# Performance work log

Measured on AMD Instinct MI355X. Metric: run time of the kernel, lower is better.

The kernel has to match this reference:

```python
import jax, jax.numpy as jnp
import numpy as np
from jax import lax

CONF_T = 0.25   # NMS.conf
IOU_T = 0.45    # NMS.iou
MAX_DET = 1000  # NMS.max_det
K_PRE = 1024    # fixed pre-NMS candidate count (static-shape surrogate for boolean filtering)
MAX_WH = 4096.0 # class offset for class-aware NMS (yolov5 trick)


def _xywh2xyxy(b):
    xy, wh = b[..., :2], b[..., 2:4]
    return jnp.concatenate([xy - wh * 0.5, xy + wh * 0.5], axis=-1)


def _box_iou(a, b):
    # a: [K,4], b: [K,4] xyxy -> [K,K]
    area_a = (a[:, 2] - a[:, 0]) * (a[:, 3] - a[:, 1])
    area_b = (b[:, 2] - b[:, 0]) * (b[:, 3] - b[:, 1])
    lt = jnp.maximum(a[:, None, :2], b[None, :, :2])
    rb = jnp.minimum(a[:, None, 2:], b[None, :, 2:])
    wh = jnp.clip(rb - lt, 0.0)
    inter = wh[..., 0] * wh[..., 1]
    return inter / (area_a[:, None] + area_b[None, :] - inter + 1e-7)


def _nms_single(p):
    # p: [N, 5+nc]
    obj = p[:, 4]
    cls_scores = p[:, 5:] * obj[:, None]          # conf = obj_conf * cls_conf
    conf = jnp.max(cls_scores, axis=-1)           # best-class confidence
    cls = jnp.argmax(cls_scores, axis=-1)
    valid = (obj > CONF_T) & (conf > CONF_T)      # candidate + conf threshold
    score = jnp.where(valid, conf, -1.0)

    top_conf, top_idx = lax.top_k(score, K_PRE)   # static pre-NMS selection
    boxes = _xywh2xyxy(p[:, :4])[top_idx]         # [K,4]
    cls_k = cls[top_idx].astype(p.dtype)
    off_boxes = boxes + (cls_k * MAX_WH)[:, None] # class-aware offset

    iou = _box_iou(off_boxes, off_boxes)          # [K,K]
    keep0 = top_conf > 0.0
    ar = jnp.arange(K_PRE)

    def body(i, keep):
        sup = (iou[i] > IOU_T) & (ar > i) & keep[i]
        return keep & ~sup

    keep = lax.fori_loop(0, K_PRE, body, keep0)

    kscore = jnp.where(keep, top_conf, -1.0)
    out_c, out_i = lax.top_k(kscore, MAX_DET)     # max_det cap
    dets = jnp.concatenate(
        [boxes[out_i], top_conf[out_i][:, None], cls_k[out_i][:, None]], axis=-1
    )                                             # [max_det, 6] (xyxy, conf, cls)
    vmask = out_c > 0.0
    dets = jnp.where(vmask[:, None], dets, 0.0)
    return dets, vmask


def setup_inputs() -> dict:
    key = jax.random.key(0)
    B, N, C = 16, 25200, 85
    x = jax.random.uniform(key, (B, N, C), dtype=jnp.float32)
    x = x.at[..., :4].multiply(640.0)  # xywh in pixel scale
    return {"x": x}


def reference(x):
    dets, vmask = jax.vmap(_nms_single)(x)
    return dets, vmask
```

## Files before the change

kernel.cpp:

```cpp
#include <hip/hip_runtime.h>
#include <cstdint>
#include <cstddef>

#define BATCH 16
#define NBOX 25200
#define NCH 85
#define KPRE 1024
#define MAXDET 1000
#define NCAND_MAX 4096
#define CSHIFT 12
#define HB 4096
#define HBASE 0x40800
#define IDX_PAD 0xFFFFFFFFu

__device__ __forceinline__ unsigned key_of(float s) {
    unsigned u = __float_as_uint(s);
    unsigned m = (u & 0x80000000u) ? ~u : (u | 0x80000000u);
    return ~m;
}

__global__ __launch_bounds__(256, 2) void score_kernel(const float* __restrict__ x,
                                                       unsigned* __restrict__ k32) {
    int gid = blockIdx.x * 256 + threadIdx.x;
    int box = gid >> 1;
    int q = gid & 1;
    size_t base = (size_t)box * NCH;

    float obj = x[base + 4];
    const float4* p = (const float4*)(x + base + 5 + q * 40);
    float4 r[10];
    #pragma unroll
    for (int j = 0; j < 10; j++) r[j] = p[j];

    float v = -1e30f;
    #pragma unroll
    for (int j = 0; j < 10; j++) {
        float m0 = fmaxf(r[j].x * obj, r[j].y * obj);
        float m1 = fmaxf(r[j].z * obj, r[j].w * obj);
        v = fmaxf(v, fmaxf(m0, m1));
    }
    v = fmaxf(v, __shfl_xor(v, 1));

    if (q == 0) {
        bool validb = (obj > 0.25f) && (v > 0.25f);
        float score = validb ? v : -1.0f;
        k32[box] = key_of(score);
    }
}

__global__ __launch_bounds__(1024) void select_cutoff(const unsigned* __restrict__ k32,
                                                      unsigned* __restrict__ cutoff) {
    __shared__ unsigned h[HB];
    __shared__ unsigned part[1024];
    __shared__ unsigned wsum[16];
    int b = blockIdx.x, t = threadIdx.x;
    int lane = t & 63, wv = t >> 6;

    #pragma unroll
    for (int j = 0; j < HB / 1024; j++) h[t + j * 1024] = 0;
    __syncthreads();

    const unsigned* kb = k32 + (size_t)b * NBOX;
    for (int i = t; i < NBOX; i += 1024) {
        unsigned k = kb[i];
        if ((int)k >= 0) {
            int bu = (int)(k >> CSHIFT) - HBASE;
            bu = bu < 0 ? 0 : (bu > HB - 1 ? HB - 1 : bu);
            atomicAdd(&h[bu], 1u);
        }
    }
    __syncthreads();

    unsigned s = h[4 * t] + h[4 * t + 1] + h[4 * t + 2] + h[4 * t + 3];
    part[t] = s;
    unsigned ws = s;
    #pragma unroll
    for (int off = 1; off < 64; off <<= 1) ws += __shfl_xor(ws, off);
    if (lane == 0) wsum[wv] = ws;
    __syncthreads();
    if (t == 0) {
        unsigned cum = 0; int W = -1;
        for (int w = 0; w < 16; w++)
            if (W < 0) { if (cum + wsum[w] >= KPRE) W = w; else cum += wsum[w]; }
        int T = -1;
        if (W >= 0)
            for (int i = 0; i < 64; i++)
                if (T < 0) { int p = W * 64 + i; if (cum + part[p] >= KPRE) T = p; else cum += part[p]; }
        unsigned P = HB - 1;
        if (T >= 0)
            for (int j = 0; j < 4; j++) { cum += h[T * 4 + j]; if (cum >= KPRE) { P = (unsigned)(T * 4 + j); break; } }
        cutoff[b] = P + HBASE;
    }
}

__global__ __launch_bounds__(1024) void sort_gather(const unsigned* __restrict__ k32,
                                                    const unsigned* __restrict__ cutoff,
                                                    float* __restrict__ topconf,
                                                    unsigned* __restrict__ topidx) {
    __shared__ unsigned long long keys[NCAND_MAX];
    __shared__ unsigned cnt[25][16];
    __shared__ unsigned waveOff[25][16];
    __shared__ unsigned chunkBase[25];
    __shared__ unsigned totc[25];
    __shared__ unsigned nTot;
    int b = blockIdx.x, t = threadIdx.x;
    int lane = t & 63, wv = t >> 6;
    unsigned P = cutoff[b];
    const unsigned* kb = k32 + (size_t)b * NBOX;

    unsigned kreg[25];
    unsigned passbits = 0;
    #pragma unroll
    for (int c = 0; c < 25; c++) {
        int i = c * 1024 + t;
        unsigned k = 0; bool p = false;
        if (i < NBOX) { k = kb[i]; p = ((int)k >= 0) && ((k >> CSHIFT) <= P); }
        kreg[c] = k;
        passbits |= (p ? 1u : 0u) << c;
    }
    #pragma unroll
    for (int c = 0; c < 25; c++) {
        unsigned long long m = __ballot((passbits >> c) & 1u);
        if (lane == 0) cnt[c][wv] = (unsigned)__popcll(m);
    }
    __syncthreads();
    if (t < 25) {
        unsigned run = 0;
        #pragma unroll
        for (int w2 = 0; w2 < 16; w2++) { waveOff[t][w2] = run; run += cnt[t][w2]; }
        totc[t] = run;
    }
    __syncthreads();
    if (t == 0) {
        unsigned acc = 0;
        for (int c = 0; c < 25; c++) { chunkBase[c] = acc; acc += totc[c]; }
        nTot = acc;
    }
    __syncthreads();
    int n = (int)nTot; if (n > NCAND_MAX) n = NCAND_MAX;
    #pragma unroll
    for (int c = 0; c < 25; c++) {
        unsigned long long m = __ballot((passbits >> c) & 1u);
        if ((passbits >> c) & 1u) {
            unsigned rank = chunkBase[c] + waveOff[c][wv] +
                            (unsigned)__popcll(lane ? (m & ((~0ull) >> (64 - lane))) : 0ull);
            if (rank < NCAND_MAX)
                keys[rank] = ((unsigned long long)kreg[c] << 32) | (unsigned)(c * 1024 + t);
        }
    }
    int m2 = KPRE;
    while (m2 < n) m2 <<= 1;
    int nq = m2 >> 10;
    for (int q = 0; q < nq; q++) { int s2 = t + (q << 10); if (s2 >= n) keys[s2] = ~0ull; }
    __syncthreads();

    for (int k = 2; k <= m2; k <<= 1) {
        for (int j = k >> 1; j > 0; j >>= 1) {
            for (int q = 0; q < nq; q++) {
                int i = t + (q << 10);
                int ixj = i ^ j;
                if (ixj > i) {
                    unsigned long long a = keys[i], bb = keys[ixj];
                    bool up = ((i & k) == 0);
                    if ((a > bb) == up) { keys[i] = bb; keys[ixj] = a; }
                }
            }
            __syncthreads();
        }
    }

    int o = (b << 10) + t;
    if (t < n) {
        unsigned long long key = keys[t];
        unsigned kk = (unsigned)(key >> 32);
        unsigned mm = ~kk;
        unsigned bits = (mm & 0x80000000u) ? (mm & 0x7FFFFFFFu) : ~mm;
        topconf[o] = __uint_as_float(bits);
        topidx[o] = (unsigned)(key & 0xFFFFFFFFu);
    } else {
        topconf[o] = -1.0f;
        topidx[o] = IDX_PAD;
    }
}

__global__ __launch_bounds__(256) void argmax_gather(const float* __restrict__ x,
                                                     const unsigned* __restrict__ topidx,
                                                     float4* __restrict__ topbox,
                                                     float4* __restrict__ topoff,
                                                     float* __restrict__ topcls) {
#pragma clang fp contract(off)
    int gid = blockIdx.x * 256 + threadIdx.x;
    int o = gid >> 2;
    int q = gid & 3;
    int b = o >> 10;
    unsigned idx = topidx[o];

    float4 box = make_float4(0.f, 0.f, 0.f, 0.f);
    float clsf = 0.f;
    if (idx != IDX_PAD) {
        size_t base = ((size_t)b * NBOX + idx) * NCH;
        float obj = x[base + 4];
        int cbase = 5 + q * 20;
        float v = -1e30f; int c = 0;
        #pragma unroll
        for (int j = 0; j < 20; j++) {
            float s = x[base + cbase + j] * obj;
            if (s > v) { v = s; c = q * 20 + j; }
        }
        #pragma unroll
        for (int off = 1; off <= 2; off <<= 1) {
            float ov = __shfl_xor(v, off);
            int   oc = __shfl_xor(c, off);
            if (ov > v || (ov == v && oc < c)) { v = ov; c = oc; }
        }
        if (q == 0) {
            float cx = x[base + 0], cy = x[base + 1], w = x[base + 2], h = x[base + 3];
            box = make_float4(cx - w * 0.5f, cy - h * 0.5f, cx + w * 0.5f, cy + h * 0.5f);
            clsf = (float)c;
        }
    }
    if (q == 0) {
        topbox[o] = box;
        topcls[o] = clsf;
        float off = clsf * 4096.0f;
        topoff[o] = make_float4(box.x + off, box.y + off, box.z + off, box.w + off);
    }
}

__global__ __launch_bounds__(256) void iou_mask(const float4* __restrict__ topoff,
                                                unsigned long long* __restrict__ mask,
                                                unsigned short* __restrict__ summ) {
#pragma clang fp contract(off)
    __shared__ float4 soff[KPRE];
    int b = blockIdx.x >> 6;
    int blk = blockIdx.x & 63;
    int t = threadIdx.x;
    for (int q = 0; q < 4; q++) {
        int u = t + q * 256;
        int s = ((u & 15) << 6) | (u >> 4);
        soff[u] = topoff[(b << 10) + s];
    }
    __syncthreads();
    int i = (blk << 4) + (t >> 4);
    int w = t & 15;
    unsigned long long bits = 0;
    int jbase = w << 6;
    if (jbase + 63 > i) {
        float4 a = soff[((i & 63) << 4) | (i >> 6)];
        float area_a = (a.z - a.x) * (a.w - a.y);
        for (int jj = 0; jj < 64; jj++) {
            int j = jbase + jj;
            float4 bb = soff[(jj << 4) | w];
            float area_b = (bb.z - bb.x) * (bb.w - bb.y);
            float ltx = fmaxf(a.x, bb.x), lty = fmaxf(a.y, bb.y);
            float rbx = fminf(a.z, bb.z), rby = fminf(a.w, bb.w);
            float wx = fmaxf(rbx - ltx, 0.0f), wy = fmaxf(rby - lty, 0.0f);
            float inter = wx * wy;
            float iou = inter / (area_a + area_b - inter + 1e-7f);
            if (j > i && iou > 0.45f) bits |= (1ull << jj);
        }
    }
    mask[((size_t)((b << 10) + i) << 4) + w] = bits;
    unsigned long long bal = __ballot(bits != 0ull);
    if (w == 0) {
        int l = t & 63;
        summ[(b << 10) + i] = (unsigned short)((bal >> ((l >> 4) << 4)) & 0xFFFFull);
    }
}

__global__ __launch_bounds__(1024) void nms_finalize(const unsigned long long* __restrict__ mask,
                                                     const unsigned short* __restrict__ summ,
                                                     const float* __restrict__ topconf,
                                                     const float4* __restrict__ topbox,
                                                     const float* __restrict__ topcls,
                                                     float* __restrict__ dets,
                                                     float* __restrict__ vmask) {
    __shared__ unsigned long long kb[16];
    int b = blockIdx.x, tid = threadIdx.x;

    if (tid < 64) {
        int lane = tid;
        const unsigned long long* mrow = mask + ((size_t)b << 14);
        unsigned long long keep0[16];
        #pragma unroll
        for (int c = 0; c < 16; c++) {
            float cf = topconf[(b << 10) + (c << 6) + lane];
            keep0[c] = __ballot(cf > 0.0f);
        }
        unsigned nz[16];
        #pragma unroll
        for (int t = 0; t < 16; t++)
            nz[t] = (unsigned)summ[(b << 10) + (t << 6) + lane];
        unsigned long long diag[16];
        #pragma unroll
        for (int t = 0; t < 16; t++)
            diag[t] = mrow[((size_t)((t << 6) + lane) << 4) + t];

        unsigned long long remv[16];
        #pragma unroll
        for (int t = 0; t < 16; t++) remv[t] = 0;

        #pragma unroll
        for (int t = 0; t < 16; t++) {
            unsigned long long live = keep0[t] & ~remv[t];
            unsigned long long kept = live;
            unsigned long long pend = live & __ballot((nz[t] >> t) & 1u);
            while (pend) {
                int j = (int)__ffsll(pend) - 1;
                pend &= pend - 1;
                if ((kept >> j) & 1ull) {
                    unsigned long long dj = __shfl(diag[t], j);
                    kept &= ~dj;
                    pend &= ~dj;
                }
            }
            if (lane == 0) kb[t] = kept;

            #pragma unroll
            for (int w = 0; w < 16; w++) {
                if (w > t) {
                    unsigned long long wm = kept & __ballot((nz[t] >> w) & 1u);
                    while (wm) {
                        int j = (int)__ffsll(wm) - 1;
                        wm &= wm - 1;
                        remv[w] |= mrow[((size_t)((t << 6) + j) << 4) + w];
                    }
                }
            }
        }
    }
    __syncthreads();

    int r = tid;
    int w = r >> 6, l = r & 63;
    unsigned long long word = kb[w];
    int keep = (int)((word >> l) & 1ull);
    int base = 0, total = 0;
    #pragma unroll
    for (int q = 0; q < 16; q++) {
        int c = __popcll(kb[q]);
        total += c;
        if (q < w) base += c;
    }
    int rank = base + __popcll((l == 0) ? 0ull : (word & ((~0ull) >> (64 - l))));
    float* drow = dets + (size_t)b * (MAXDET * 6);
    float* vm = vmask + (size_t)b * MAXDET;
    if (r < MAXDET && r >= total) {
#pragma unroll
        for (int cc = 0; cc < 6; cc++) drow[r * 6 + cc] = 0.0f;
        vm[r] = 0.0f;
    }
    if (keep && rank < MAXDET) {
        int o = (b << 10) + r;
        float4 bx = topbox[o];
        drow[rank * 6 + 0] = bx.x;
        drow[rank * 6 + 1] = bx.y;
        drow[rank * 6 + 2] = bx.z;
        drow[rank * 6 + 3] = bx.w;
        drow[rank * 6 + 4] = topconf[o];
        drow[rank * 6 + 5] = topcls[o];
        vm[rank] = 1.0f;
    }
}

extern "C" void kernel_launch(void* const* d_in, const int* in_sizes, int n_in,
                              void* d_out, int out_size, void* d_ws, size_t ws_size,
                              hipStream_t stream) {
    const float* x = (const float*)d_in[0];
    char* w = (char*)d_ws;

    unsigned long long* mask    = (unsigned long long*)(w + 0);
    unsigned*           k32     = (unsigned*)(w + 2097152);
    float4*             topbox  = (float4*)(w + 3709952);
    float4*             topoff  = (float4*)(w + 3972096);
    float*              topconf = (float*)(w + 4234240);
    float*              topcls  = (float*)(w + 4299776);
    unsigned*           topidx  = (unsigned*)(w + 4365312);
    unsigned*           cutoff  = (unsigned*)(w + 4430848);
    unsigned short*     summ    = (unsigned short*)(w + 4430912);
    if (ws_size < 4463808) return;

    score_kernel<<<(BATCH * NBOX * 2) / 256, 256, 0, stream>>>(x, k32);
    select_cutoff<<<BATCH, 1024, 0, stream>>>(k32, cutoff);
    sort_gather<<<BATCH, 1024, 0, stream>>>(k32, cutoff, topconf, topidx);
    argmax_gather<<<(BATCH * KPRE * 4) / 256, 256, 0, stream>>>(x, topidx, topbox, topoff, topcls);
    iou_mask<<<BATCH * 64, 256, 0, stream>>>(topoff, mask, summ);

    float* dets = (float*)d_out;
    float* vmask = dets + (size_t)BATCH * MAXDET * 6;
    nms_finalize<<<BATCH, 1024, 0, stream>>>(mask, summ, topconf, topbox, topcls, dets, vmask);
}
```

Baseline: 111.3 us.

## Fuse histogram cutoff into sort_gather and widen score kernel to four lanes per box

The cutoff histogram kernel is merged into the sort/gather kernel, so the per-batch keys are loaded once into registers and reused for both the histogram and the compaction, which removes a launch and a second read of k32. The score kernel now gives each box to four threads using aligned float4 loads over the whole row, masking out the non-class lanes, and takes the max of the raw class scores before a single multiply by obj. The fused kernel uses more shared memory and more registers per block, and taking max before multiplying is only equivalent because obj is positive whenever the threshold passes.

New measurement: 104.4 us. 6.3% less time.

```diff
diff --git a/kernel.cpp b/kernel.cpp
--- a/kernel.cpp
+++ b/kernel.cpp
@@ -19,64 +19,91 @@
     return ~m;
 }
 
-__global__ __launch_bounds__(256, 2) void score_kernel(const float* __restrict__ x,
-                                                       unsigned* __restrict__ k32) {
+__global__ __launch_bounds__(256) void score_kernel(const float* __restrict__ x,
+                                                    unsigned* __restrict__ k32) {
     int gid = blockIdx.x * 256 + threadIdx.x;
-    int box = gid >> 1;
-    int q = gid & 1;
-    size_t base = (size_t)box * NCH;
-
-    float obj = x[base + 4];
-    const float4* p = (const float4*)(x + base + 5 + q * 40);
-    float4 r[10];
-    #pragma unroll
-    for (int j = 0; j < 10; j++) r[j] = p[j];
-
-    float v = -1e30f;
-    #pragma unroll
-    for (int j = 0; j < 10; j++) {
-        float m0 = fmaxf(r[j].x * obj, r[j].y * obj);
-        float m1 = fmaxf(r[j].z * obj, r[j].w * obj);
-        v = fmaxf(v, fmaxf(m0, m1));
-    }
+    int box = gid >> 2;
+    int q = gid & 3;
+    const float* rowp = x + (size_t)box * NCH;
+
+    float obj = rowp[4];
+    const float4* p4 = (const float4*)rowp;
+    float4 r0 = p4[q];
+    float4 r1 = p4[q + 4];
+    float4 r2 = p4[q + 8];
+    float4 r3 = p4[q + 12];
+    float4 r4 = p4[q + 16];
+    float4 rt = p4[20];
+    float c79 = rowp[84];
+
+    if (q == 0) { r0.x = -1e30f; r0.y = -1e30f; r0.z = -1e30f; r0.w = -1e30f; }
+    if (q == 1) { r0.x = -1e30f; }
+
+    float v = fmaxf(fmaxf(r0.x, r0.y), fmaxf(r0.z, r0.w));
+    v = fmaxf(v, fmaxf(fmaxf(r1.x, r1.y), fmaxf(r1.z, r1.w)));
+    v = fmaxf(v, fmaxf(fmaxf(r2.x, r2.y), fmaxf(r2.z, r2.w)));
+    v = fmaxf(v, fmaxf(fmaxf(r3.x, r3.y), fmaxf(r3.z, r3.w)));
+    v = fmaxf(v, fmaxf(fmaxf(r4.x, r4.y), fmaxf(r4.z, r4.w)));
+    v = fmaxf(v, fmaxf(fmaxf(rt.x, rt.y), fmaxf(rt.z, rt.w)));
+    v = fmaxf(v, c79);
     v = fmaxf(v, __shfl_xor(v, 1));
+    v = fmaxf(v, __shfl_xor(v, 2));
 
     if (q == 0) {
-        bool validb = (obj > 0.25f) && (v > 0.25f);
-        float score = validb ? v : -1.0f;
-        k32[box] = key_of(score);
-    }
-}
-
-__global__ __launch_bounds__(1024) void select_cutoff(const unsigned* __restrict__ k32,
-                                                      unsigned* __restrict__ cutoff) {
+        float conf = obj * v;
+        bool validb = (obj > 0.25f) && (conf > 0.25f);
+        k32[box] = key_of(validb ? conf : -1.0f);
+    }
+}
+
+__global__ __launch_bounds__(1024) void sort_gather(const unsigned* __restrict__ k32,
+                                                    float* __restrict__ topconf,
+                                                    unsigned* __restrict__ topidx) {
+    __shared__ unsigned long long keys[NCAND_MAX];
     __shared__ unsigned h[HB];
     __shared__ unsigned part[1024];
     __shared__ unsigned wsum[16];
+    __shared__ unsigned cnt[25][16];
+    __shared__ unsigned waveOff[25][16];
+    __shared__ unsigned chunkBase[25];
+    __shared__ unsigned totc[25];
+    __shared__ unsigned cutP, nTot;
     int b = blockIdx.x, t = threadIdx.x;
     int lane = t & 63, wv = t >> 6;
+    const unsigned* kb = k32 + (size_t)b * NBOX;
+
+    unsigned kreg[25];
+    unsigned validbits = 0;
+    #pragma unroll
+    for (int c = 0; c < 25; c++) {
+        int i = c * 1024 + t;
+        unsigned k = 0x80000000u;
+        if (i < NBOX) k = kb[i];
+        kreg[c] = k;
+        validbits |= (((int)k >= 0) ? 1u : 0u) << c;
+    }
 
     #pragma unroll
     for (int j = 0; j < HB / 1024; j++) h[t + j * 1024] = 0;
     __syncthreads();
-
-    const unsigned* kb = k32 + (size_t)b * NBOX;
-    for (int i = t; i < NBOX; i += 1024) {
-        unsigned k = kb[i];
-        if ((int)k >= 0) {
-            int bu = (int)(k >> CSHIFT) - HBASE;
+    #pragma unroll
+    for (int c = 0; c < 25; c++) {
+        if ((validbits >> c) & 1u) {
+            int bu = (int)(kreg[c] >> CSHIFT) - HBASE;
             bu = bu < 0 ? 0 : (bu > HB - 1 ? HB - 1 : bu);
             atomicAdd(&h[bu], 1u);
         }
     }
     __syncthreads();
 
-    unsigned s = h[4 * t] + h[4 * t + 1] + h[4 * t + 2] + h[4 * t + 3];
-    part[t] = s;
-    unsigned ws = s;
-    #pragma unroll
-    for (int off = 1; off < 64; off <<= 1) ws += __shfl_xor(ws, off);
-    if (lane == 0) wsum[wv] = ws;
+    {
+        unsigned s = h[4 * t] + h[4 * t + 1] + h[4 * t + 2] + h[4 * t + 3];
+        part[t] = s;
+        unsigned ws = s;
+        #pragma unroll
+        for (int off = 1; off < 64; off <<= 1) ws += __shfl_xor(ws, off);
+        if (lane == 0) wsum[wv] = ws;
+    }
     __syncthreads();
     if (t == 0) {
         unsigned cum = 0; int W = -1;
@@ -89,33 +116,15 @@
         unsigned P = HB - 1;
         if (T >= 0)
             for (int j = 0; j < 4; j++) { cum += h[T * 4 + j]; if (cum >= KPRE) { P = (unsigned)(T * 4 + j); break; } }
-        cutoff[b] = P + HBASE;
-    }
-}
-
-__global__ __launch_bounds__(1024) void sort_gather(const unsigned* __restrict__ k32,
-                                                    const unsigned* __restrict__ cutoff,
-                                                    float* __restrict__ topconf,
-                                                    unsigned* __restrict__ topidx) {
-    __shared__ unsigned long long keys[NCAND_MAX];
-    __shared__ unsigned cnt[25][16];
-    __shared__ unsigned waveOff[25][16];
-    __shared__ unsigned chunkBase[25];
-    __shared__ unsigned totc[25];
-    __shared__ unsigned nTot;
-    int b = blockIdx.x, t = threadIdx.x;
-    int lane = t & 63, wv = t >> 6;
-    unsigned P = cutoff[b];
-    const unsigned* kb = k32 + (size_t)b * NBOX;
-
-    unsigned kreg[25];
+        cutP = P + HBASE;
+    }
+    __syncthreads();
+    unsigned P = cutP;
+
     unsigned passbits = 0;
     #pragma unroll
     for (int c = 0; c < 25; c++) {
-        int i = c * 1024 + t;
-        unsigned k = 0; bool p = false;
-        if (i < NBOX) { k = kb[i]; p = ((int)k >= 0) && ((k >> CSHIFT) <= P); }
-        kreg[c] = k;
+        bool p = ((validbits >> c) & 1u) && ((kreg[c] >> CSHIFT) <= P);
         passbits |= (p ? 1u : 0u) << c;
     }
     #pragma unroll
@@ -376,13 +385,11 @@
     float*              topconf = (float*)(w + 4234240);
     float*              topcls  = (float*)(w + 4299776);
     unsigned*           topidx  = (unsigned*)(w + 4365312);
-    unsigned*           cutoff  = (unsigned*)(w + 4430848);
-    unsigned short*     summ    = (unsigned short*)(w + 4430912);
-    if (ws_size < 4463808) return;
-
-    score_kernel<<<(BATCH * NBOX * 2) / 256, 256, 0, stream>>>(x, k32);
-    select_cutoff<<<BATCH, 1024, 0, stream>>>(k32, cutoff);
-    sort_gather<<<BATCH, 1024, 0, stream>>>(k32, cutoff, topconf, topidx);
+    unsigned short*     summ    = (unsigned short*)(w + 4430848);
+    if (ws_size < 4463616) return;
+
+    score_kernel<<<(BATCH * NBOX * 4) / 256, 256, 0, stream>>>(x, k32);
+    sort_gather<<<BATCH, 1024, 0, stream>>>(k32, topconf, topidx);
     argmax_gather<<<(BATCH * KPRE * 4) / 256, 256, 0, stream>>>(x, topidx, topbox, topoff, topcls);
     iou_mask<<<BATCH * 64, 256, 0, stream>>>(topoff, mask, summ);
 
```
